# Kernel tuning notes

Measured on AMD Instinct MI355X. Metric: run time of the kernel, lower is better.

Reference implementation:

```python
import jax, jax.numpy as jnp
import numpy as np

NUM_CLASSES = 151  # Visual Genome object classes
PRED_DIM = 51      # predicate distribution channels (50 predicates + bg)


def _conv2d(x, w, pad):
    # x: [B, Cin, H, W], w: [Cout, Cin, kh, kw]
    return jax.lax.conv_general_dilated(
        x, w, window_strides=(1, 1), padding=[(pad, pad), (pad, pad)],
        dimension_numbers=("NCHW", "OIHW", "NCHW"))


def setup_inputs() -> dict:
    key = jax.random.key(0)
    ks = jax.random.split(key, 12)
    B, N, D = 64, 80, 4096
    K = D // 4  # 1024
    s = 0.02
    return {
        "encoder_reps": jax.random.normal(ks[0], (B, N, D), jnp.float32),
        "obj_preds": jax.random.randint(ks[1], (B, N), 0, NUM_CLASSES, jnp.int32),
        "freq_table": jax.random.normal(ks[2], (NUM_CLASSES * NUM_CLASSES, PRED_DIM), jnp.float32),
        "W_comp": jax.random.normal(ks[3], (D, K), jnp.float32) * s,
        "W_ou1": jax.random.normal(ks[4], (K, K), jnp.float32) * s,
        "W_ofc": jax.random.normal(ks[5], (K, K), jnp.float32) * s,
        "W_decomp": jax.random.normal(ks[6], (K, D), jnp.float32) * s,
        "conv1": jax.random.normal(ks[7], (10, PRED_DIM, 3, 3), jnp.float32) * s,
        "conv2": jax.random.normal(ks[8], (5, 10, 3, 3), jnp.float32) * s,
        "conv3": jax.random.normal(ks[9], (1, 5, 1, 1), jnp.float32) * s,
    }


def reference(encoder_reps, obj_preds, freq_table, W_comp, W_ou1, W_ofc,
              W_decomp, conv1, conv2, conv3):
    B, N, D = encoder_reps.shape
    # obj_comp: Linear(D, D//4, bias=False) + ReLU
    comp = jax.nn.relu(jnp.einsum("bnd,dk->bnk", encoder_reps, W_comp))  # [B,N,K]
    # ou1: Linear(K, K, bias=False) + ReLU
    obj_u1 = jax.nn.relu(jnp.einsum("bnk,kj->bnj", comp, W_ou1))          # [B,N,K]
    # pairwise product indices -> freq_bias.index_with_labels (subj*C + obj)
    pair_idx = obj_preds[:, :, None] * NUM_CLASSES + obj_preds[:, None, :]  # [B,N,N]
    rel_u1 = freq_table[pair_idx]                                          # [B,N,N,51]
    # adjacency via small conv stack + sigmoid
    x = jnp.transpose(rel_u1, (0, 3, 1, 2))      # [B,51,N,N]
    x = _conv2d(x, conv1, pad=1)                 # [B,10,N,N]
    x = _conv2d(x, conv2, pad=1)                 # [B,5,N,N]
    x = _conv2d(x, conv3, pad=0)                 # [B,1,N,N]
    adj = jax.nn.sigmoid(x[:, 0])                # [B,N,N]
    # normalized Laplacian: D^-1/2 (A + I) D^-1/2
    A_hat = adj + jnp.eye(N, dtype=adj.dtype)[None]
    d = (jnp.sum(A_hat, axis=2) + 1e-5) ** (-0.5)                          # [B,N]
    L_hat = d[:, :, None] * A_hat * d[:, None, :]                          # [B,N,N]
    ofl_u = jnp.einsum("bnm,bmk->bnk", L_hat, obj_u1)                      # [B,N,K]
    # ofc_u + obj_decomp + residual
    u_m = jax.nn.relu(jnp.einsum("bnk,kj->bnj", ofl_u, W_ofc))
    decomp = jax.nn.relu(jnp.einsum("bnk,kd->bnd", u_m, W_decomp))
    return decomp + encoder_reps
```

## Files before the change

kernel.cpp:

```cpp
#include <hip/hip_runtime.h>
#include <hip/hip_bf16.h>
#include <math.h>

typedef __bf16 bf16x8 __attribute__((ext_vector_type(8)));
typedef float floatx4 __attribute__((ext_vector_type(4)));
typedef float float4v __attribute__((ext_vector_type(4)));
typedef float float2v __attribute__((ext_vector_type(2)));
typedef unsigned short ushortx4 __attribute__((ext_vector_type(4)));
typedef unsigned short ushortx8 __attribute__((ext_vector_type(8)));

__device__ __forceinline__ unsigned short f2bf(float f) {
    unsigned int u = __builtin_bit_cast(unsigned int, f);
    u += 0x7FFFu + ((u >> 16) & 1u);
    return (unsigned short)(u >> 16);
}
__device__ __forceinline__ float bf2f(unsigned short h) {
    unsigned int u = ((unsigned int)h) << 16;
    return __builtin_bit_cast(float, u);
}

__device__ __forceinline__ void gload_lds16(const void* g, void* l) {
    __builtin_amdgcn_global_load_lds(
        (const __attribute__((address_space(1))) unsigned int*)g,
        (__attribute__((address_space(3))) unsigned int*)l, 16, 0, 0);
}

__global__ __launch_bounds__(256) void cast_bf16_kernel(
    const float* __restrict__ in, unsigned short* __restrict__ out, long n8)
{
    long i = (long)blockIdx.x * 256 + threadIdx.x;
    long stride = (long)gridDim.x * 256;
    for (; i < n8; i += stride) {
        float4v a = reinterpret_cast<const float4v*>(in)[2 * i];
        float4v b = reinterpret_cast<const float4v*>(in)[2 * i + 1];
        ushortx8 h;
        #pragma unroll
        for (int q = 0; q < 4; ++q) { h[q] = f2bf(a[q]); h[4 + q] = f2bf(b[q]); }
        reinterpret_cast<ushortx8*>(out)[i] = h;
    }
}

__global__ __launch_bounds__(256) void reduce3_kernel(
    const unsigned short* __restrict__ p0, const unsigned short* __restrict__ p1,
    const unsigned short* __restrict__ p2, unsigned short* __restrict__ out,
    long n8)
{
    long i = (long)blockIdx.x * 256 + threadIdx.x;
    long stride = (long)gridDim.x * 256;
    const ushortx8* a0 = reinterpret_cast<const ushortx8*>(p0);
    const ushortx8* a1 = reinterpret_cast<const ushortx8*>(p1);
    const ushortx8* a2 = reinterpret_cast<const ushortx8*>(p2);
    for (; i < n8; i += stride) {
        ushortx8 x = a0[i], y = a1[i], zv = a2[i];
        ushortx8 h;
        #pragma unroll
        for (int q = 0; q < 8; ++q)
            h[q] = f2bf(fmaxf(bf2f(x[q]) + bf2f(y[q]) + bf2f(zv[q]), 0.0f));
        reinterpret_cast<ushortx8*>(out)[i] = h;
    }
}

__global__ __launch_bounds__(256) void prep_kernel(
    const float* __restrict__ w1, const float* __restrict__ w2,
    const float* __restrict__ w3, float* __restrict__ W1e,
    float* __restrict__ w23)
{
    for (int idx = threadIdx.x; idx < 4590; idx += 256) {
        int ci = idx / 90, rem = idx % 90;
        int tap = rem / 10, co = rem % 10;
        int di = tap / 3, dj = tap % 3;
        W1e[idx] = w1[((co * 51 + ci) * 3 + di) * 3 + dj];
    }
    if (threadIdx.x < 90) {
        int tap = threadIdx.x / 10, c10 = threadIdx.x % 10;
        int di = tap / 3, dj = tap % 3;
        float s = 0.f;
        #pragma unroll
        for (int c5 = 0; c5 < 5; ++c5)
            s = fmaf(w3[c5], w2[((c5 * 10 + c10) * 3 + di) * 3 + dj], s);
        w23[threadIdx.x] = s;
    }
}

__global__ __launch_bounds__(256) void fp1_kernel(
    const float* __restrict__ freq, const float* __restrict__ W1e,
    float* __restrict__ Fp1)
{
    __shared__ float W1s[4590];
    for (int idx = threadIdx.x; idx < 4590; idx += 256)
        W1s[idx] = W1e[idx];
    __syncthreads();
    int p = blockIdx.x * 256 + threadIdx.x;
    if (p >= 22801) return;
    float2v acc[45];
    #pragma unroll
    for (int t = 0; t < 45; ++t) { acc[t][0] = 0.f; acc[t][1] = 0.f; }
    const float* fr = freq + (size_t)p * 51;
    for (int ci = 0; ci < 51; ++ci) {
        float v = fr[ci];
        const float2v* wrow = reinterpret_cast<const float2v*>(&W1s[ci * 90]);
        #pragma unroll
        for (int t = 0; t < 45; ++t) {
            float2v w = wrow[t];
            acc[t][0] = fmaf(v, w[0], acc[t][0]);
            acc[t][1] = fmaf(v, w[1], acc[t][1]);
        }
    }
    float2v* out = reinterpret_cast<float2v*>(Fp1 + (size_t)p * 90);
    #pragma unroll
    for (int t = 0; t < 45; ++t) out[t] = acc[t];
}

__global__ __launch_bounds__(320) void gather_kernel(
    const int* __restrict__ preds, const float* __restrict__ Fp1,
    float* __restrict__ h1)
{
    __shared__ int pb[80];
    const int b = blockIdx.y;
    const int tid = threadIdx.x;
    if (tid < 80) pb[tid] = preds[b * 80 + tid];
    __syncthreads();
    const int i = blockIdx.x * 4 + tid / 80;
    const int j = tid % 80;
    float2v acc[5];
    #pragma unroll
    for (int q = 0; q < 5; ++q) { acc[q][0] = 0.f; acc[q][1] = 0.f; }
    #pragma unroll
    for (int di = 0; di < 3; ++di) {
        int ii = i + di - 1;
        if (ii < 0 || ii >= 80) continue;
        int pi = pb[ii] * 151;
        #pragma unroll
        for (int dj = 0; dj < 3; ++dj) {
            int jj = j + dj - 1;
            if (jj < 0 || jj >= 80) continue;
            const float2v* row = reinterpret_cast<const float2v*>(
                Fp1 + (size_t)(pi + pb[jj]) * 90 + (di * 3 + dj) * 10);
            #pragma unroll
            for (int q = 0; q < 5; ++q) {
                float2v v = row[q];
                acc[q][0] += v[0];
                acc[q][1] += v[1];
            }
        }
    }
    float2v* out = reinterpret_cast<float2v*>(
        h1 + ((size_t)b * 6400 + i * 80 + j) * 10);
    #pragma unroll
    for (int q = 0; q < 5; ++q) out[q] = acc[q];
}

__global__ __launch_bounds__(320) void conv23_kernel(
    const float* __restrict__ h1, const float* __restrict__ w23g,
    float* __restrict__ adj)
{
    __shared__ float w23s[90];
    const int tid = threadIdx.x;
    if (tid < 90) w23s[tid] = w23g[tid];
    __syncthreads();
    const int b = blockIdx.y;
    const int i = blockIdx.x * 4 + tid / 80;
    const int j = tid % 80;
    float t = 0.f;
    #pragma unroll
    for (int di = 0; di < 3; ++di) {
        int ii = i + di - 1;
        if (ii < 0 || ii >= 80) continue;
        #pragma unroll
        for (int dj = 0; dj < 3; ++dj) {
            int jj = j + dj - 1;
            if (jj < 0 || jj >= 80) continue;
            const float2v* hp = reinterpret_cast<const float2v*>(
                h1 + ((size_t)b * 6400 + ii * 80 + jj) * 10);
            const float* wp = w23s + (di * 3 + dj) * 10;
            #pragma unroll
            for (int q = 0; q < 5; ++q) {
                float2v v = hp[q];
                t = fmaf(v[0], wp[2 * q], t);
                t = fmaf(v[1], wp[2 * q + 1], t);
            }
        }
    }
    adj[(size_t)b * 6400 + i * 80 + j] = 1.0f / (1.0f + __expf(-t));
}

__global__ __launch_bounds__(128) void degree_kernel(
    const float* __restrict__ adj, float* __restrict__ deg)
{
    int b = blockIdx.x;
    int i = threadIdx.x;
    if (i >= 80) return;
    const float* row = adj + (size_t)b * 6400 + i * 80;
    float s = 1.0f + 1e-5f;
    for (int jj = 0; jj < 80; ++jj) s += row[jj];
    deg[b * 80 + i] = rsqrtf(s);
}

__global__ __launch_bounds__(256) void transpose_cast(
    const float* __restrict__ in, unsigned short* __restrict__ out,
    int R, int C)
{
    __shared__ float t[32][33];
    const int tx = threadIdx.x & 31;
    const int ty = threadIdx.x >> 5;
    const int r0 = blockIdx.y * 32, c0 = blockIdx.x * 32;
    #pragma unroll
    for (int k = 0; k < 4; ++k)
        t[ty + k * 8][tx] = in[(size_t)(r0 + ty + k * 8) * C + c0 + tx];
    __syncthreads();
    #pragma unroll
    for (int k = 0; k < 4; ++k)
        out[(size_t)(c0 + ty + k * 8) * R + r0 + tx] = f2bf(t[tx][ty + k * 8]);
}

template<int MODE>
__global__ __launch_bounds__(512, 1) void gemm8(
    const unsigned short* __restrict__ Ap, const unsigned short* __restrict__ Bt,
    void* __restrict__ Cp, const float* __restrict__ Rp,
    unsigned short* __restrict__ P1, unsigned short* __restrict__ P2,
    int M, int N, int lda, int khA, int khB)
{
    __shared__ __align__(16) unsigned short S[65536];
    auto Apl = [&](int buf, int ks) { return S + (buf * 2 + ks) * 8192; };
    auto Bpl = [&](int buf, int ks) { return S + 32768 + (buf * 2 + ks) * 8192; };

    const int tid = threadIdx.x;
    const int bm  = blockIdx.x * 256;
    const int bn  = blockIdx.y * 256;
    const int z   = blockIdx.z;
    const int k0  = z ? (khA + (z - 1) * khB) : 0;
    const int kh  = z ? khB : khA;
    const int nt  = kh >> 6;

    const int w    = tid >> 6;
    const int lane = tid & 63;
    const int wr   = w >> 2;
    const int wc   = w & 3;
    const int lr   = lane & 15;
    const int lo   = lane >> 4;
    const int r3   = lr & 3;
    const int soct = (lo ^ r3) * 8;

    floatx4 acc[8][4];
    #pragma unroll
    for (int i = 0; i < 8; ++i)
        #pragma unroll
        for (int j = 0; j < 4; ++j)
            #pragma unroll
            for (int r = 0; r < 4; ++r) acc[i][j][r] = 0.0f;

    auto stageA = [&](int buf, int ks, int kt) {
        #pragma unroll
        for (int it = 0; it < 2; ++it) {
            int d = tid + it * 512;
            int row = d >> 2, s = d & 3;
            gload_lds16(
                &Ap[(size_t)(bm + row) * lda + kt + ks * 32 + ((s ^ (row & 3)) * 8)],
                &Apl(buf, ks)[d * 8]);
        }
    };
    auto stageB = [&](int buf, int ks, int kt) {
        #pragma unroll
        for (int it = 0; it < 2; ++it) {
            int d = tid + it * 512;
            int row = d >> 2, s = d & 3;
            gload_lds16(
                &Bt[(size_t)(bn + row) * lda + kt + ks * 32 + ((s ^ (row & 3)) * 8)],
                &Bpl(buf, ks)[d * 8]);
        }
    };

    stageA(0, 0, k0); stageB(0, 0, k0); stageA(0, 1, k0); stageB(0, 1, k0);

    for (int t = 0; t < nt; ++t) {
        const int cur = t & 1;
        const int nxt = cur ^ 1;
        const int ktn = k0 + ((t + 1) << 6);
        const bool pf = (t + 1 < nt);

        asm volatile("s_waitcnt vmcnt(4)" ::: "memory");
        __builtin_amdgcn_s_barrier();
        __builtin_amdgcn_sched_barrier(0);
        bf16x8 b0[4], af[4];
        #pragma unroll
        for (int n = 0; n < 4; ++n)
            b0[n] = *reinterpret_cast<const bf16x8*>(
                &Bpl(cur, 0)[(wc * 64 + n * 16 + lr) * 32 + soct]);
        #pragma unroll
        for (int m = 0; m < 4; ++m)
            af[m] = *reinterpret_cast<const bf16x8*>(
                &Apl(cur, 0)[(wr * 128 + m * 16 + lr) * 32 + soct]);
        if (pf) stageA(nxt, 0, ktn);
        __builtin_amdgcn_s_setprio(1);
        #pragma unroll
        for (int m = 0; m < 4; ++m)
            #pragma unroll
            for (int n = 0; n < 4; ++n)
                acc[m][n] = __builtin_amdgcn_mfma_f32_16x16x32_bf16(
                    b0[n], af[m], acc[m][n], 0, 0, 0);
        __builtin_amdgcn_s_setprio(0);

        #pragma unroll
        for (int m = 0; m < 4; ++m)
            af[m] = *reinterpret_cast<const bf16x8*>(
                &Apl(cur, 0)[(wr * 128 + (m + 4) * 16 + lr) * 32 + soct]);
        if (pf) stageB(nxt, 0, ktn);
        __builtin_amdgcn_s_setprio(1);
        #pragma unroll
        for (int m = 0; m < 4; ++m)
            #pragma unroll
            for (int n = 0; n < 4; ++n)
                acc[m + 4][n] = __builtin_amdgcn_mfma_f32_16x16x32_bf16(
                    b0[n], af[m], acc[m + 4][n], 0, 0, 0);
        __builtin_amdgcn_s_setprio(0);

        if (pf) { asm volatile("s_waitcnt vmcnt(4)" ::: "memory"); }
        else    { asm volatile("s_waitcnt vmcnt(0)" ::: "memory"); }
        __builtin_amdgcn_s_barrier();
        __builtin_amdgcn_sched_barrier(0);
        #pragma unroll
        for (int n = 0; n < 4; ++n)
            b0[n] = *reinterpret_cast<const bf16x8*>(
                &Bpl(cur, 1)[(wc * 64 + n * 16 + lr) * 32 + soct]);
        #pragma unroll
        for (int m = 0; m < 4; ++m)
            af[m] = *reinterpret_cast<const bf16x8*>(
                &Apl(cur, 1)[(wr * 128 + m * 16 + lr) * 32 + soct]);
        if (pf) stageA(nxt, 1, ktn);
        __builtin_amdgcn_s_setprio(1);
        #pragma unroll
        for (int m = 0; m < 4; ++m)
            #pragma unroll
            for (int n = 0; n < 4; ++n)
                acc[m][n] = __builtin_amdgcn_mfma_f32_16x16x32_bf16(
                    b0[n], af[m], acc[m][n], 0, 0, 0);
        __builtin_amdgcn_s_setprio(0);

        #pragma unroll
        for (int m = 0; m < 4; ++m)
            af[m] = *reinterpret_cast<const bf16x8*>(
                &Apl(cur, 1)[(wr * 128 + (m + 4) * 16 + lr) * 32 + soct]);
        if (pf) stageB(nxt, 1, ktn);
        __builtin_amdgcn_s_setprio(1);
        #pragma unroll
        for (int m = 0; m < 4; ++m)
            #pragma unroll
            for (int n = 0; n < 4; ++n)
                acc[m + 4][n] = __builtin_amdgcn_mfma_f32_16x16x32_bf16(
                    b0[n], af[m], acc[m + 4][n], 0, 0, 0);
        __builtin_amdgcn_s_setprio(0);
    }

    __syncthreads();

    if (MODE == 2) {
        #pragma unroll
        for (int mi = 0; mi < 8; ++mi) {
            const int mrow = wr * 128 + mi * 16 + lr;
            const int swz = (mrow & 7) << 4;
            #pragma unroll
            for (int ni = 0; ni < 4; ++ni) {
                const int ncol = wc * 64 + ni * 16 + lo * 4;
                ushortx4 v;
                #pragma unroll
                for (int rr = 0; rr < 4; ++rr) v[rr] = f2bf(acc[mi][ni][rr]);
                *reinterpret_cast<ushortx4*>(
                    (char*)S + ((mrow * 512 + ncol * 2) ^ swz)) = v;
            }
        }
        __syncthreads();
        unsigned short* dst =
            (z == 0) ? (unsigned short*)Cp : ((z == 1) ? P1 : P2);
        #pragma unroll
        for (int it = 0; it < 16; ++it) {
            int idx = tid + it * 512;
            int r = idx >> 5, c = idx & 31;
            ushortx8 v = *reinterpret_cast<const ushortx8*>(
                (char*)S + ((r * 512 + c * 16) ^ ((r & 7) << 4)));
            *reinterpret_cast<ushortx8*>(
                &dst[(size_t)(bm + r) * N + bn + c * 8]) = v;
        }
    } else {
        #pragma unroll
        for (int p = 0; p < 2; ++p) {
            if ((wc >> 1) == p) {
                #pragma unroll
                for (int mi = 0; mi < 8; ++mi) {
                    const int mrow = wr * 128 + mi * 16 + lr;
                    const int swz = (mrow & 7) << 4;
                    #pragma unroll
                    for (int ni = 0; ni < 4; ++ni) {
                        const int nc = (wc & 1) * 64 + ni * 16 + lo * 4;
                        float4v v;
                        #pragma unroll
                        for (int rr = 0; rr < 4; ++rr) v[rr] = acc[mi][ni][rr];
                        *reinterpret_cast<float4v*>(
                            (char*)S + ((mrow * 512 + nc * 4) ^ swz)) = v;
                    }
                }
            }
            __syncthreads();
            #pragma unroll
            for (int it = 0; it < 16; ++it) {
                int idx = tid + it * 512;
                int r = idx >> 5, c = idx & 31;
                float4v v = *reinterpret_cast<const float4v*>(
                    (char*)S + ((r * 512 + c * 16) ^ ((r & 7) << 4)));
                size_t off = (size_t)(bm + r) * N + bn + p * 128 + c * 4;
                float4v rv = *reinterpret_cast<const float4v*>(&Rp[off]);
                float4v o;
                #pragma unroll
                for (int rr = 0; rr < 4; ++rr)
                    o[rr] = fmaxf(v[rr], 0.f) + rv[rr];
                *reinterpret_cast<float4v*>(&((float*)Cp)[off]) = o;
            }
            if (p == 0) __syncthreads();
        }
    }
}

__global__ __launch_bounds__(256) void gemm_pipe0(
    const unsigned short* __restrict__ Ap, const unsigned short* __restrict__ Bt,
    unsigned short* __restrict__ Cp, int M, int N, int lda)
{
    __shared__ unsigned short Al[2][128 * 32];
    __shared__ unsigned short Bl[2][128 * 32];
    const int tid  = threadIdx.x;
    const int bm   = blockIdx.x * 128;
    const int bn   = blockIdx.y * 128;
    const int wave = tid >> 6;
    const int lane = tid & 63;
    const int wm   = (wave >> 1) * 64;
    const int wn   = (wave & 1) * 64;
    const int lr   = lane & 15;
    const int lk   = (lane >> 4) * 8;
    floatx4 acc[4][4];
    #pragma unroll
    for (int i = 0; i < 4; ++i)
        #pragma unroll
        for (int j = 0; j < 4; ++j)
            #pragma unroll
            for (int r = 0; r < 4; ++r) acc[i][j][r] = 0.0f;
    auto stage = [&](int buf, int kq) {
        #pragma unroll
        for (int it = 0; it < 2; ++it) {
            int idx = tid + it * 256;
            gload_lds16(&Ap[(size_t)(bm + (idx >> 2)) * lda + kq + (idx & 3) * 8],
                        &Al[buf][idx * 8]);
        }
        #pragma unroll
        for (int it = 0; it < 2; ++it) {
            int idx = tid + it * 256;
            gload_lds16(&Bt[(size_t)(bn + (idx >> 2)) * lda + kq + (idx & 3) * 8],
                        &Bl[buf][idx * 8]);
        }
    };
    stage(0, 0);
    __syncthreads();
    const int nt = lda >> 5;
    int cur = 0;
    for (int t = 0; t < nt; ++t) {
        if (t + 1 < nt) stage(cur ^ 1, (t + 1) << 5);
        bf16x8 af[4], bfv[4];
        #pragma unroll
        for (int mi = 0; mi < 4; ++mi)
            af[mi] = *reinterpret_cast<const bf16x8*>(
                &Al[cur][(wm + mi * 16 + lr) * 32 + lk]);
        #pragma unroll
        for (int ni = 0; ni < 4; ++ni)
            bfv[ni] = *reinterpret_cast<const bf16x8*>(
                &Bl[cur][(wn + ni * 16 + lr) * 32 + lk]);
        #pragma unroll
        for (int mi = 0; mi < 4; ++mi)
            #pragma unroll
            for (int ni = 0; ni < 4; ++ni)
                acc[mi][ni] = __builtin_amdgcn_mfma_f32_16x16x32_bf16(
                    af[mi], bfv[ni], acc[mi][ni], 0, 0, 0);
        __syncthreads();
        cur ^= 1;
    }
    #pragma unroll
    for (int mi = 0; mi < 4; ++mi)
        #pragma unroll
        for (int ni = 0; ni < 4; ++ni)
            #pragma unroll
            for (int r = 0; r < 4; ++r) {
                int row = bm + wm + mi * 16 + (lane >> 4) * 4 + r;
                int col = bn + wn + ni * 16 + lr;
                Cp[(size_t)row * N + col] = f2bf(fmaxf(acc[mi][ni][r], 0.f));
            }
}

__global__ __launch_bounds__(256) void gemm_f32a(
    const float* __restrict__ Ap, const unsigned short* __restrict__ Bt,
    unsigned short* __restrict__ Cp, int M, int N, int lda)
{
    __shared__ unsigned short Al[2][128 * 40];
    __shared__ unsigned short Bl[2][128 * 32];
    const int tid  = threadIdx.x;
    const int bm   = blockIdx.x * 128;
    const int bn   = blockIdx.y * 128;
    const int wave = tid >> 6;
    const int lane = tid & 63;
    const int wm   = (wave >> 1) * 64;
    const int wn   = (wave & 1) * 64;
    const int lr   = lane & 15;
    const int lk   = (lane >> 4) * 8;
    floatx4 acc[4][4];
    #pragma unroll
    for (int i = 0; i < 4; ++i)
        #pragma unroll
        for (int j = 0; j < 4; ++j)
            #pragma unroll
            for (int r = 0; r < 4; ++r) acc[i][j][r] = 0.0f;
    auto stage = [&](int buf, int k0) {
        #pragma unroll
        for (int it = 0; it < 4; ++it) {
            int idx = tid + it * 256;
            int r = idx >> 3, kc = (idx & 7) * 4;
            float4v v = *reinterpret_cast<const float4v*>(
                &Ap[(size_t)(bm + r) * lda + k0 + kc]);
            ushortx4 h;
            #pragma unroll
            for (int q = 0; q < 4; ++q) h[q] = f2bf(v[q]);
            *reinterpret_cast<ushortx4*>(&Al[buf][r * 40 + kc]) = h;
        }
        #pragma unroll
        for (int it = 0; it < 2; ++it) {
            int idx = tid + it * 256;
            gload_lds16(&Bt[(size_t)(bn + (idx >> 2)) * lda + k0 + (idx & 3) * 8],
                        &Bl[buf][idx * 8]);
        }
    };
    stage(0, 0);
    __syncthreads();
    const int nt = lda >> 5;
    int cur = 0;
    for (int t = 0; t < nt; ++t) {
        if (t + 1 < nt) stage(cur ^ 1, (t + 1) << 5);
        bf16x8 af[4], bfv[4];
        #pragma unroll
        for (int mi = 0; mi < 4; ++mi)
            af[mi] = *reinterpret_cast<const bf16x8*>(
                &Al[cur][(wm + mi * 16 + lr) * 40 + lk]);
        #pragma unroll
        for (int ni = 0; ni < 4; ++ni)
            bfv[ni] = *reinterpret_cast<const bf16x8*>(
                &Bl[cur][(wn + ni * 16 + lr) * 32 + lk]);
        #pragma unroll
        for (int mi = 0; mi < 4; ++mi)
            #pragma unroll
            for (int ni = 0; ni < 4; ++ni)
                acc[mi][ni] = __builtin_amdgcn_mfma_f32_16x16x32_bf16(
                    af[mi], bfv[ni], acc[mi][ni], 0, 0, 0);
        __syncthreads();
        cur ^= 1;
    }
    #pragma unroll
    for (int mi = 0; mi < 4; ++mi)
        #pragma unroll
        for (int ni = 0; ni < 4; ++ni)
            #pragma unroll
            for (int r = 0; r < 4; ++r) {
                int row = bm + wm + mi * 16 + (lane >> 4) * 4 + r;
                int col = bn + wn + ni * 16 + lr;
                Cp[(size_t)row * N + col] = f2bf(fmaxf(acc[mi][ni][r], 0.f));
            }
}

__global__ __launch_bounds__(256) void laplacian_kernel(
    const float* __restrict__ adj, const float* __restrict__ deg,
    const unsigned short* __restrict__ u_in, unsigned short* __restrict__ ofl)
{
    __shared__ float wl[6400];
    __shared__ unsigned short ul[80 * 256];
    const int b   = blockIdx.y;
    const int kq  = blockIdx.x;
    const int tid = threadIdx.x;
    const int ko  = tid & 31;
    const int ngrp = tid >> 5;

    const float* ab = adj + (size_t)b * 6400;
    const float* db = deg + b * 80;
    for (int idx = tid; idx < 6400; idx += 256) {
        int n = idx / 80;
        int m = idx - n * 80;
        float w = ab[idx] + (n == m ? 1.0f : 0.0f);
        wl[idx] = w * db[m];
    }
    const unsigned short* ub = u_in + (size_t)b * 80 * 1024 + kq * 256;
    #pragma unroll
    for (int it = 0; it < 10; ++it) {
        int idx = tid + it * 256;
        int m   = idx >> 5;
        int c8  = (idx & 31) * 8;
        *reinterpret_cast<ushortx8*>(&ul[m * 256 + c8]) =
            *reinterpret_cast<const ushortx8*>(&ub[(size_t)m * 1024 + c8]);
    }
    __syncthreads();

    float acc[10][8];
    #pragma unroll
    for (int ni = 0; ni < 10; ++ni)
        #pragma unroll
        for (int q = 0; q < 8; ++q) acc[ni][q] = 0.0f;

    for (int m = 0; m < 80; ++m) {
        ushortx8 uv = *reinterpret_cast<const ushortx8*>(&ul[m * 256 + ko * 8]);
        float uf[8];
        #pragma unroll
        for (int q = 0; q < 8; ++q) uf[q] = bf2f(uv[q]);
        #pragma unroll
        for (int ni = 0; ni < 10; ++ni) {
            float wv = wl[(ngrp * 10 + ni) * 80 + m];
            #pragma unroll
            for (int q = 0; q < 8; ++q)
                acc[ni][q] = fmaf(wv, uf[q], acc[ni][q]);
        }
    }
    #pragma unroll
    for (int ni = 0; ni < 10; ++ni) {
        int n = ngrp * 10 + ni;
        float dn = db[n];
        ushortx8 o;
        #pragma unroll
        for (int q = 0; q < 8; ++q) o[q] = f2bf(acc[ni][q] * dn);
        *reinterpret_cast<ushortx8*>(
            &ofl[((size_t)(b * 80 + n)) * 1024 + kq * 256 + ko * 8]) = o;
    }
}

extern "C" void kernel_launch(void* const* d_in, const int* in_sizes, int n_in,
                              void* d_out, int out_size, void* d_ws, size_t ws_size,
                              hipStream_t stream)
{
    const float* enc   = (const float*)d_in[0];
    const int*   preds = (const int*)d_in[1];
    const float* freq  = (const float*)d_in[2];
    const float* Wc    = (const float*)d_in[3];
    const float* Wou1  = (const float*)d_in[4];
    const float* Wofc  = (const float*)d_in[5];
    const float* Wdec  = (const float*)d_in[6];
    const float* w1    = (const float*)d_in[7];
    const float* w2    = (const float*)d_in[8];
    const float* w3    = (const float*)d_in[9];

    const int M = 5120;
    const size_t SLAB = (size_t)M * 1024;
    unsigned short* comp  = (unsigned short*)d_ws;
    unsigned short* obju  = comp + SLAB;
    unsigned short* r1    = obju + SLAB;
    unsigned short* oflu  = r1;
    float*          h1    = (float*)r1;
    unsigned short* r2    = r1 + 8192000;
    unsigned short* um    = r2;
    float*          Fp1   = (float*)r2;
    unsigned short* Wcb   = r2 + SLAB;
    unsigned short* Wou1b = Wcb + (size_t)1024 * 4096;
    unsigned short* Wofcb = Wou1b + (size_t)1024 * 1024;
    unsigned short* Wdecb = Wofcb + (size_t)1024 * 1024;
    float*          W1e   = (float*)(Wdecb + (size_t)4096 * 1024);
    float*          w23   = W1e + 4590;
    float*          adj   = w23 + 90;
    float*          deg   = adj + (size_t)64 * 6400;
    unsigned short* encb  = (unsigned short*)(deg + 5120);
    const size_t need_bytes =
        ((size_t)(encb - comp) + (size_t)M * 4096) * sizeof(unsigned short);
    const bool use_encb = ws_size >= need_bytes;
    unsigned short* Q0 = encb;
    unsigned short* Q1 = encb + SLAB;
    unsigned short* Q2 = encb + 2 * SLAB;

    prep_kernel<<<1, 256, 0, stream>>>(w1, w2, w3, W1e, w23);
    transpose_cast<<<dim3(32, 128), 256, 0, stream>>>(Wc, Wcb, 4096, 1024);
    transpose_cast<<<dim3(32, 32), 256, 0, stream>>>(Wou1, Wou1b, 1024, 1024);
    transpose_cast<<<dim3(32, 32), 256, 0, stream>>>(Wofc, Wofcb, 1024, 1024);
    transpose_cast<<<dim3(128, 32), 256, 0, stream>>>(Wdec, Wdecb, 1024, 4096);

    fp1_kernel<<<90, 256, 0, stream>>>(freq, W1e, Fp1);
    gather_kernel<<<dim3(20, 64), 320, 0, stream>>>(preds, Fp1, h1);
    conv23_kernel<<<dim3(20, 64), 320, 0, stream>>>(h1, w23, adj);
    degree_kernel<<<64, 128, 0, stream>>>(adj, deg);

    if (use_encb) {
        cast_bf16_kernel<<<2048, 256, 0, stream>>>(enc, encb, (long)M * 4096 / 8);
        gemm8<2><<<dim3(20, 4, 3), 512, 0, stream>>>(
            encb, Wcb, r1, nullptr, r2, obju, M, 1024, 4096, 1408, 1344);
        reduce3_kernel<<<2048, 256, 0, stream>>>(r1, r2, obju, comp, SLAB / 8);
        gemm8<2><<<dim3(20, 4, 3), 512, 0, stream>>>(
            comp, Wou1b, Q0, nullptr, Q1, Q2, M, 1024, 1024, 384, 320);
        reduce3_kernel<<<2048, 256, 0, stream>>>(Q0, Q1, Q2, obju, SLAB / 8);
    } else {
        gemm_f32a<<<dim3(40, 8), 256, 0, stream>>>(enc, Wcb, comp, M, 1024, 4096);
        gemm_pipe0<<<dim3(40, 8), 256, 0, stream>>>(comp, Wou1b, obju, M, 1024, 1024);
    }
    laplacian_kernel<<<dim3(4, 64), 256, 0, stream>>>(adj, deg, obju, oflu);
    if (use_encb) {
        gemm8<2><<<dim3(20, 4, 3), 512, 0, stream>>>(
            oflu, Wofcb, Q0, nullptr, Q1, Q2, M, 1024, 1024, 384, 320);
        reduce3_kernel<<<2048, 256, 0, stream>>>(Q0, Q1, Q2, um, SLAB / 8);
    } else {
        gemm_pipe0<<<dim3(40, 8), 256, 0, stream>>>(oflu, Wofcb, um, M, 1024, 1024);
    }
    gemm8<1><<<dim3(20, 16, 1), 512, 0, stream>>>(
        um, Wdecb, d_out, enc, nullptr, nullptr, M, 4096, 1024, 1024, 0);
}
```

Before: 329.3 us.

## Replace 256x256 split-K GEMM with 128x128 tiles and drop split-K for square GEMMs

Swaps the 512-thread 256x256 GEMM kernel, with its three-way split-K and separate reduce passes, for a simpler 256-thread 128x128 double-buffered kernel. The first GEMM now uses a two-way split, and the K=1024 GEMMs run without any split, with ReLU fused into the epilogue. This removes two reduce kernels and their partial-buffer traffic. The final GEMM now reads the bf16 copy of the encoder input as the residual, which halves residual read bandwidth but adds the output by a bf16-rounded value. The new kernel drops the interleaved prefetch, priority hints and fine-grained waitcnt scheduling, so it may get lower MFMA utilisation.

```diff
diff --git a/kernel.cpp b/kernel.cpp
--- a/kernel.cpp
+++ b/kernel.cpp
@@ -40,22 +40,20 @@
     }
 }
 
-__global__ __launch_bounds__(256) void reduce3_kernel(
+__global__ __launch_bounds__(256) void reduce_relu_kernel(
     const unsigned short* __restrict__ p0, const unsigned short* __restrict__ p1,
-    const unsigned short* __restrict__ p2, unsigned short* __restrict__ out,
-    long n8)
+    unsigned short* __restrict__ out, long n8)
 {
     long i = (long)blockIdx.x * 256 + threadIdx.x;
     long stride = (long)gridDim.x * 256;
     const ushortx8* a0 = reinterpret_cast<const ushortx8*>(p0);
     const ushortx8* a1 = reinterpret_cast<const ushortx8*>(p1);
-    const ushortx8* a2 = reinterpret_cast<const ushortx8*>(p2);
     for (; i < n8; i += stride) {
-        ushortx8 x = a0[i], y = a1[i], zv = a2[i];
+        ushortx8 x = a0[i], y = a1[i];
         ushortx8 h;
         #pragma unroll
         for (int q = 0; q < 8; ++q)
-            h[q] = f2bf(fmaxf(bf2f(x[q]) + bf2f(y[q]) + bf2f(zv[q]), 0.0f));
+            h[q] = f2bf(fmaxf(bf2f(x[q]) + bf2f(y[q]), 0.0f));
         reinterpret_cast<ushortx8*>(out)[i] = h;
     }
 }
@@ -214,204 +212,139 @@
 }
 
 template<int MODE>
-__global__ __launch_bounds__(512, 1) void gemm8(
+__global__ __launch_bounds__(256) void gemm128(
     const unsigned short* __restrict__ Ap, const unsigned short* __restrict__ Bt,
-    void* __restrict__ Cp, const float* __restrict__ Rp,
-    unsigned short* __restrict__ P1, unsigned short* __restrict__ P2,
-    int M, int N, int lda, int khA, int khB)
-{
-    __shared__ __align__(16) unsigned short S[65536];
-    auto Apl = [&](int buf, int ks) { return S + (buf * 2 + ks) * 8192; };
-    auto Bpl = [&](int buf, int ks) { return S + 32768 + (buf * 2 + ks) * 8192; };
-
-    const int tid = threadIdx.x;
-    const int bm  = blockIdx.x * 256;
-    const int bn  = blockIdx.y * 256;
-    const int z   = blockIdx.z;
-    const int k0  = z ? (khA + (z - 1) * khB) : 0;
-    const int kh  = z ? khB : khA;
-    const int nt  = kh >> 6;
-
-    const int w    = tid >> 6;
+    void* __restrict__ Cp, const unsigned short* __restrict__ Rb,
+    unsigned short* __restrict__ P1,
+    int M, int N, int lda, int kh)
+{
+    __shared__ __align__(16) unsigned short SS[16384];
+    unsigned short* Al = SS;
+    unsigned short* Bl = SS + 8192;
+
+    const int tid  = threadIdx.x;
+    const int bm   = blockIdx.x * 128;
+    const int bn   = blockIdx.y * 128;
+    const int k0   = blockIdx.z * kh;
+    const int wave = tid >> 6;
     const int lane = tid & 63;
-    const int wr   = w >> 2;
-    const int wc   = w & 3;
+    const int wm   = (wave >> 1) * 64;
+    const int wn   = (wave & 1) * 64;
     const int lr   = lane & 15;
     const int lo   = lane >> 4;
-    const int r3   = lr & 3;
-    const int soct = (lo ^ r3) * 8;
-
-    floatx4 acc[8][4];
-    #pragma unroll
-    for (int i = 0; i < 8; ++i)
+    const int soct = (lo ^ (lr & 3)) * 8;
+
+    floatx4 acc[4][4];
+    #pragma unroll
+    for (int i = 0; i < 4; ++i)
         #pragma unroll
         for (int j = 0; j < 4; ++j)
             #pragma unroll
             for (int r = 0; r < 4; ++r) acc[i][j][r] = 0.0f;
 
-    auto stageA = [&](int buf, int ks, int kt) {
+    auto stage = [&](int buf, int kq) {
         #pragma unroll
         for (int it = 0; it < 2; ++it) {
-            int d = tid + it * 512;
-            int row = d >> 2, s = d & 3;
-            gload_lds16(
-                &Ap[(size_t)(bm + row) * lda + kt + ks * 32 + ((s ^ (row & 3)) * 8)],
-                &Apl(buf, ks)[d * 8]);
+            int idx = tid + it * 256;
+            int r = idx >> 2, s = idx & 3;
+            gload_lds16(&Ap[(size_t)(bm + r) * lda + kq + ((s ^ (r & 3)) * 8)],
+                        &Al[buf * 4096 + idx * 8]);
+        }
+        #pragma unroll
+        for (int it = 0; it < 2; ++it) {
+            int idx = tid + it * 256;
+            int r = idx >> 2, s = idx & 3;
+            gload_lds16(&Bt[(size_t)(bn + r) * lda + kq + ((s ^ (r & 3)) * 8)],
+                        &Bl[buf * 4096 + idx * 8]);
         }
     };
-    auto stageB = [&](int buf, int ks, int kt) {
-        #pragma unroll
-        for (int it = 0; it < 2; ++it) {
-            int d = tid + it * 512;
-            int row = d >> 2, s = d & 3;
-            gload_lds16(
-                &Bt[(size_t)(bn + row) * lda + kt + ks * 32 + ((s ^ (row & 3)) * 8)],
-                &Bpl(buf, ks)[d * 8]);
-        }
-    };
-
-    stageA(0, 0, k0); stageB(0, 0, k0); stageA(0, 1, k0); stageB(0, 1, k0);
-
+
+    stage(0, k0);
+    __syncthreads();
+    const int nt = kh >> 5;
+    int cur = 0;
     for (int t = 0; t < nt; ++t) {
-        const int cur = t & 1;
-        const int nxt = cur ^ 1;
-        const int ktn = k0 + ((t + 1) << 6);
-        const bool pf = (t + 1 < nt);
-
-        asm volatile("s_waitcnt vmcnt(4)" ::: "memory");
-        __builtin_amdgcn_s_barrier();
-        __builtin_amdgcn_sched_barrier(0);
-        bf16x8 b0[4], af[4];
-        #pragma unroll
-        for (int n = 0; n < 4; ++n)
-            b0[n] = *reinterpret_cast<const bf16x8*>(
-                &Bpl(cur, 0)[(wc * 64 + n * 16 + lr) * 32 + soct]);
-        #pragma unroll
-        for (int m = 0; m < 4; ++m)
-            af[m] = *reinterpret_cast<const bf16x8*>(
-                &Apl(cur, 0)[(wr * 128 + m * 16 + lr) * 32 + soct]);
-        if (pf) stageA(nxt, 0, ktn);
-        __builtin_amdgcn_s_setprio(1);
-        #pragma unroll
-        for (int m = 0; m < 4; ++m)
-            #pragma unroll
-            for (int n = 0; n < 4; ++n)
-                acc[m][n] = __builtin_amdgcn_mfma_f32_16x16x32_bf16(
-                    b0[n], af[m], acc[m][n], 0, 0, 0);
-        __builtin_amdgcn_s_setprio(0);
-
-        #pragma unroll
-        for (int m = 0; m < 4; ++m)
-            af[m] = *reinterpret_cast<const bf16x8*>(
-                &Apl(cur, 0)[(wr * 128 + (m + 4) * 16 + lr) * 32 + soct]);
-        if (pf) stageB(nxt, 0, ktn);
-        __builtin_amdgcn_s_setprio(1);
-        #pragma unroll
-        for (int m = 0; m < 4; ++m)
-            #pragma unroll
-            for (int n = 0; n < 4; ++n)
-                acc[m + 4][n] = __builtin_amdgcn_mfma_f32_16x16x32_bf16(
-                    b0[n], af[m], acc[m + 4][n], 0, 0, 0);
-        __builtin_amdgcn_s_setprio(0);
-
-        if (pf) { asm volatile("s_waitcnt vmcnt(4)" ::: "memory"); }
-        else    { asm volatile("s_waitcnt vmcnt(0)" ::: "memory"); }
-        __builtin_amdgcn_s_barrier();
-        __builtin_amdgcn_sched_barrier(0);
-        #pragma unroll
-        for (int n = 0; n < 4; ++n)
-            b0[n] = *reinterpret_cast<const bf16x8*>(
-                &Bpl(cur, 1)[(wc * 64 + n * 16 + lr) * 32 + soct]);
-        #pragma unroll
-        for (int m = 0; m < 4; ++m)
-            af[m] = *reinterpret_cast<const bf16x8*>(
-                &Apl(cur, 1)[(wr * 128 + m * 16 + lr) * 32 + soct]);
-        if (pf) stageA(nxt, 1, ktn);
-        __builtin_amdgcn_s_setprio(1);
-        #pragma unroll
-        for (int m = 0; m < 4; ++m)
-            #pragma unroll
-            for (int n = 0; n < 4; ++n)
-                acc[m][n] = __builtin_amdgcn_mfma_f32_16x16x32_bf16(
-                    b0[n], af[m], acc[m][n], 0, 0, 0);
-        __builtin_amdgcn_s_setprio(0);
-
-        #pragma unroll
-        for (int m = 0; m < 4; ++m)
-            af[m] = *reinterpret_cast<const bf16x8*>(
-                &Apl(cur, 1)[(wr * 128 + (m + 4) * 16 + lr) * 32 + soct]);
-        if (pf) stageB(nxt, 1, ktn);
-        __builtin_amdgcn_s_setprio(1);
-        #pragma unroll
-        for (int m = 0; m < 4; ++m)
-            #pragma unroll
-            for (int n = 0; n < 4; ++n)
-                acc[m + 4][n] = __builtin_amdgcn_mfma_f32_16x16x32_bf16(
-                    b0[n], af[m], acc[m + 4][n], 0, 0, 0);
-        __builtin_amdgcn_s_setprio(0);
-    }
-
-    __syncthreads();
-
-    if (MODE == 2) {
-        #pragma unroll
-        for (int mi = 0; mi < 8; ++mi) {
-            const int mrow = wr * 128 + mi * 16 + lr;
+        if (t + 1 < nt) stage(cur ^ 1, k0 + ((t + 1) << 5));
+        bf16x8 af[4], bfv[4];
+        #pragma unroll
+        for (int mi = 0; mi < 4; ++mi)
+            af[mi] = *reinterpret_cast<const bf16x8*>(
+                &Al[cur * 4096 + (wm + mi * 16 + lr) * 32 + soct]);
+        #pragma unroll
+        for (int ni = 0; ni < 4; ++ni)
+            bfv[ni] = *reinterpret_cast<const bf16x8*>(
+                &Bl[cur * 4096 + (wn + ni * 16 + lr) * 32 + soct]);
+        #pragma unroll
+        for (int mi = 0; mi < 4; ++mi)
+            #pragma unroll
+            for (int ni = 0; ni < 4; ++ni)
+                acc[mi][ni] = __builtin_amdgcn_mfma_f32_16x16x32_bf16(
+                    bfv[ni], af[mi], acc[mi][ni], 0, 0, 0);
+        __syncthreads();
+        cur ^= 1;
+    }
+
+    if (MODE == 0 || MODE == 2) {
+        #pragma unroll
+        for (int mi = 0; mi < 4; ++mi) {
+            const int mrow = wm + mi * 16 + lr;
             const int swz = (mrow & 7) << 4;
             #pragma unroll
             for (int ni = 0; ni < 4; ++ni) {
-                const int ncol = wc * 64 + ni * 16 + lo * 4;
+                const int nc = wn + ni * 16 + lo * 4;
                 ushortx4 v;
                 #pragma unroll
-                for (int rr = 0; rr < 4; ++rr) v[rr] = f2bf(acc[mi][ni][rr]);
+                for (int rr = 0; rr < 4; ++rr)
+                    v[rr] = f2bf(MODE == 0 ? fmaxf(acc[mi][ni][rr], 0.f)
+                                           : acc[mi][ni][rr]);
                 *reinterpret_cast<ushortx4*>(
-                    (char*)S + ((mrow * 512 + ncol * 2) ^ swz)) = v;
+                    (char*)SS + ((mrow * 256 + nc * 2) ^ swz)) = v;
             }
         }
         __syncthreads();
-        unsigned short* dst =
-            (z == 0) ? (unsigned short*)Cp : ((z == 1) ? P1 : P2);
-        #pragma unroll
-        for (int it = 0; it < 16; ++it) {
-            int idx = tid + it * 512;
-            int r = idx >> 5, c = idx & 31;
+        unsigned short* dst = (MODE == 2 && blockIdx.z)
+            ? P1 : (unsigned short*)Cp;
+        #pragma unroll
+        for (int it = 0; it < 8; ++it) {
+            int idx = tid + it * 256;
+            int r = idx >> 4, c = idx & 15;
             ushortx8 v = *reinterpret_cast<const ushortx8*>(
-                (char*)S + ((r * 512 + c * 16) ^ ((r & 7) << 4)));
+                (char*)SS + ((r * 256 + c * 16) ^ ((r & 7) << 4)));
             *reinterpret_cast<ushortx8*>(
                 &dst[(size_t)(bm + r) * N + bn + c * 8]) = v;
         }
     } else {
         #pragma unroll
         for (int p = 0; p < 2; ++p) {
-            if ((wc >> 1) == p) {
+            if ((wave & 1) == p) {
                 #pragma unroll
-                for (int mi = 0; mi < 8; ++mi) {
-                    const int mrow = wr * 128 + mi * 16 + lr;
+                for (int mi = 0; mi < 4; ++mi) {
+                    const int mrow = wm + mi * 16 + lr;
                     const int swz = (mrow & 7) << 4;
                     #pragma unroll
                     for (int ni = 0; ni < 4; ++ni) {
-                        const int nc = (wc & 1) * 64 + ni * 16 + lo * 4;
+                        const int nc = ni * 16 + lo * 4;
                         float4v v;
                         #pragma unroll
                         for (int rr = 0; rr < 4; ++rr) v[rr] = acc[mi][ni][rr];
                         *reinterpret_cast<float4v*>(
-                            (char*)S + ((mrow * 512 + nc * 4) ^ swz)) = v;
+                            (char*)SS + ((mrow * 256 + nc * 4) ^ swz)) = v;
                     }
                 }
             }
             __syncthreads();
             #pragma unroll
-            for (int it = 0; it < 16; ++it) {
-                int idx = tid + it * 512;
-                int r = idx >> 5, c = idx & 31;
+            for (int it = 0; it < 8; ++it) {
+                int idx = tid + it * 256;
+                int r = idx >> 4, c = idx & 15;
                 float4v v = *reinterpret_cast<const float4v*>(
-                    (char*)S + ((r * 512 + c * 16) ^ ((r & 7) << 4)));
-                size_t off = (size_t)(bm + r) * N + bn + p * 128 + c * 4;
-                float4v rv = *reinterpret_cast<const float4v*>(&Rp[off]);
+                    (char*)SS + ((r * 256 + c * 16) ^ ((r & 7) << 4)));
+                size_t off = (size_t)(bm + r) * N + bn + p * 64 + c * 4;
+                ushortx4 rv = *reinterpret_cast<const ushortx4*>(&Rb[off]);
                 float4v o;
                 #pragma unroll
                 for (int rr = 0; rr < 4; ++rr)
-                    o[rr] = fmaxf(v[rr], 0.f) + rv[rr];
+                    o[rr] = fmaxf(v[rr], 0.f) + bf2f(rv[rr]);
                 *reinterpret_cast<float4v*>(&((float*)Cp)[off]) = o;
             }
             if (p == 0) __syncthreads();
@@ -565,6 +498,79 @@
                 int row = bm + wm + mi * 16 + (lane >> 4) * 4 + r;
                 int col = bn + wn + ni * 16 + lr;
                 Cp[(size_t)row * N + col] = f2bf(fmaxf(acc[mi][ni][r], 0.f));
+            }
+}
+
+__global__ __launch_bounds__(256) void gemm_res_f32(
+    const unsigned short* __restrict__ Ap, const unsigned short* __restrict__ Bt,
+    float* __restrict__ Cp, const float* __restrict__ Rp, int M, int N, int lda)
+{
+    __shared__ unsigned short Al[2][128 * 32];
+    __shared__ unsigned short Bl[2][128 * 32];
+    const int tid  = threadIdx.x;
+    const int bm   = blockIdx.x * 128;
+    const int bn   = blockIdx.y * 128;
+    const int wave = tid >> 6;
+    const int lane = tid & 63;
+    const int wm   = (wave >> 1) * 64;
+    const int wn   = (wave & 1) * 64;
+    const int lr   = lane & 15;
+    const int lk   = (lane >> 4) * 8;
+    floatx4 acc[4][4];
+    #pragma unroll
+    for (int i = 0; i < 4; ++i)
+        #pragma unroll
+        for (int j = 0; j < 4; ++j)
+            #pragma unroll
+            for (int r = 0; r < 4; ++r) acc[i][j][r] = 0.0f;
+    auto stage = [&](int buf, int kq) {
+        #pragma unroll
+        for (int it = 0; it < 2; ++it) {
+            int idx = tid + it * 256;
+            gload_lds16(&Ap[(size_t)(bm + (idx >> 2)) * lda + kq + (idx & 3) * 8],
+                        &Al[buf][idx * 8]);
+        }
+        #pragma unroll
+        for (int it = 0; it < 2; ++it) {
+            int idx = tid + it * 256;
+            gload_lds16(&Bt[(size_t)(bn + (idx >> 2)) * lda + kq + (idx & 3) * 8],
+                        &Bl[buf][idx * 8]);
+        }
+    };
+    stage(0, 0);
+    __syncthreads();
+    const int nt = lda >> 5;
+    int cur = 0;
+    for (int t = 0; t < nt; ++t) {
+        if (t + 1 < nt) stage(cur ^ 1, (t + 1) << 5);
+        bf16x8 af[4], bfv[4];
+        #pragma unroll
+        for (int mi = 0; mi < 4; ++mi)
+            af[mi] = *reinterpret_cast<const bf16x8*>(
+                &Al[cur][(wm + mi * 16 + lr) * 32 + lk]);
+        #pragma unroll
+        for (int ni = 0; ni < 4; ++ni)
+            bfv[ni] = *reinterpret_cast<const bf16x8*>(
+                &Bl[cur][(wn + ni * 16 + lr) * 32 + lk]);
+        #pragma unroll
+        for (int mi = 0; mi < 4; ++mi)
+            #pragma unroll
+            for (int ni = 0; ni < 4; ++ni)
+                acc[mi][ni] = __builtin_amdgcn_mfma_f32_16x16x32_bf16(
+                    af[mi], bfv[ni], acc[mi][ni], 0, 0, 0);
+        __syncthreads();
+        cur ^= 1;
+    }
+    #pragma unroll
+    for (int mi = 0; mi < 4; ++mi)
+        #pragma unroll
+        for (int ni = 0; ni < 4; ++ni)
+            #pragma unroll
+            for (int r = 0; r < 4; ++r) {
+                int row = bm + wm + mi * 16 + (lane >> 4) * 4 + r;
+                int col = bn + wn + ni * 16 + lr;
+                size_t off = (size_t)row * N + col;
+                Cp[off] = fmaxf(acc[mi][ni][r], 0.f) + Rp[off];
             }
 }
 
@@ -667,9 +673,6 @@
     const size_t need_bytes =
         ((size_t)(encb - comp) + (size_t)M * 4096) * sizeof(unsigned short);
     const bool use_encb = ws_size >= need_bytes;
-    unsigned short* Q0 = encb;
-    unsigned short* Q1 = encb + SLAB;
-    unsigned short* Q2 = encb + 2 * SLAB;
 
     prep_kernel<<<1, 256, 0, stream>>>(w1, w2, w3, W1e, w23);
     transpose_cast<<<dim3(32, 128), 256, 0, stream>>>(Wc, Wcb, 4096, 1024);
@@ -684,24 +687,24 @@
 
     if (use_encb) {
         cast_bf16_kernel<<<2048, 256, 0, stream>>>(enc, encb, (long)M * 4096 / 8);
-        gemm8<2><<<dim3(20, 4, 3), 512, 0, stream>>>(
-            encb, Wcb, r1, nullptr, r2, obju, M, 1024, 4096, 1408, 1344);
-        reduce3_kernel<<<2048, 256, 0, stream>>>(r1, r2, obju, comp, SLAB / 8);
-        gemm8<2><<<dim3(20, 4, 3), 512, 0, stream>>>(
-            comp, Wou1b, Q0, nullptr, Q1, Q2, M, 1024, 1024, 384, 320);
-        reduce3_kernel<<<2048, 256, 0, stream>>>(Q0, Q1, Q2, obju, SLAB / 8);
+        gemm128<2><<<dim3(40, 8, 2), 256, 0, stream>>>(
+            encb, Wcb, r1, nullptr, r2, M, 1024, 4096, 2048);
+        reduce_relu_kernel<<<2048, 256, 0, stream>>>(r1, r2, comp, SLAB / 8);
+        gemm128<0><<<dim3(40, 8, 1), 256, 0, stream>>>(
+            comp, Wou1b, obju, nullptr, nullptr, M, 1024, 1024, 1024);
     } else {
         gemm_f32a<<<dim3(40, 8), 256, 0, stream>>>(enc, Wcb, comp, M, 1024, 4096);
         gemm_pipe0<<<dim3(40, 8), 256, 0, stream>>>(comp, Wou1b, obju, M, 1024, 1024);
     }
     laplacian_kernel<<<dim3(4, 64), 256, 0, stream>>>(adj, deg, obju, oflu);
     if (use_encb) {
-        gemm8<2><<<dim3(20, 4, 3), 512, 0, stream>>>(
-            oflu, Wofcb, Q0, nullptr, Q1, Q2, M, 1024, 1024, 384, 320);
-        reduce3_kernel<<<2048, 256, 0, stream>>>(Q0, Q1, Q2, um, SLAB / 8);
+        gemm128<0><<<dim3(40, 8, 1), 256, 0, stream>>>(
+            oflu, Wofcb, um, nullptr, nullptr, M, 1024, 1024, 1024);
+        gemm128<1><<<dim3(40, 32, 1), 256, 0, stream>>>(
+            um, Wdecb, d_out, encb, nullptr, M, 4096, 1024, 1024);
     } else {
         gemm_pipe0<<<dim3(40, 8), 256, 0, stream>>>(oflu, Wofcb, um, M, 1024, 1024);
-    }
-    gemm8<1><<<dim3(20, 16, 1), 512, 0, stream>>>(
-        um, Wdecb, d_out, enc, nullptr, nullptr, M, 4096, 1024, 1024, 0);
-}
+        gemm_res_f32<<<dim3(40, 32), 256, 0, stream>>>(
+            um, Wdecb, (float*)d_out, enc, M, 4096, 1024);
+    }
+}
```

Measured after the change: 321.3 us. 2.4% less time.
